# Kernel optimization log

Measured on AMD Instinct MI355X. Metric: run time of the kernel, lower is better.

## Reference

```python
import jax, jax.numpy as jnp
import numpy as np
from jax import lax

COST_BBOX = 1.0  # matcher weight on the L1 bbox cost
INF = jnp.float32(1e9)


def setup_inputs() -> dict:
    key = jax.random.key(0)
    k1, k2 = jax.random.split(key)
    # [bs, num_queries, 2] predicted point coords, [bs, num_targets, 2] gt coords
    outputs = jax.random.uniform(k1, (8, 512, 2), dtype=jnp.float32)
    targets = jax.random.uniform(k2, (8, 256, 2), dtype=jnp.float32)
    return {"outputs": outputs, "targets": targets}


def _hungarian(cost):
    """Jonker-Volgenant / shortest-augmenting-path Hungarian.

    cost: [T, Q] with T <= Q. Assigns each of the T workers (targets) a
    distinct column (query) minimizing total cost. Returns
    (row_ind [T] sorted query indices, col_ind [T] matched target indices),
    matching scipy.optimize.linear_sum_assignment on cost.T.
    """
    T, Q = cost.shape
    u0 = jnp.zeros((T,), cost.dtype)            # worker potentials
    v0 = jnp.zeros((Q + 1,), cost.dtype)        # column potentials (+1 virtual col)
    p0 = jnp.full((Q + 1,), -1, jnp.int32)      # p[j] = worker assigned to column j

    def assign_one(i, carry):
        u, v, p = carry
        p = p.at[Q].set(i)                      # virtual column holds current worker
        init = (jnp.int32(Q), u, v, p,
                jnp.full((Q,), INF, cost.dtype),  # minv: tentative reduced dists
                jnp.zeros((Q + 1,), bool),        # used columns
                jnp.zeros((Q,), jnp.int32))       # way: predecessor column

        def cond(st):
            j0, _, _, p, _, _, _ = st
            return p[j0] != -1

        def body(st):
            j0, u, v, p, minv, used, way = st
            used = used.at[j0].set(True)
            i0 = p[j0]
            cur = cost[i0] - u[i0] - v[:Q]
            better = (cur < minv) & (~used[:Q])
            minv = jnp.where(better, cur, minv)
            way = jnp.where(better, j0, way)
            masked = jnp.where(used[:Q], INF, minv)
            j1 = jnp.argmin(masked).astype(jnp.int32)
            delta = masked[j1]
            uf = used.astype(cost.dtype)
            u = u.at[jnp.where(used, p, T)].add(delta * uf, mode="drop")
            v = v - delta * uf
            minv = jnp.where(used[:Q], minv, minv - delta)
            return (j1, u, v, p, minv, used, way)

        j0, u, v, p, minv, used, way = lax.while_loop(cond, body, init)

        # augment along the alternating path back to the virtual column
        def aug_cond(st):
            j0, _ = st
            return j0 != Q

        def aug_body(st):
            j0, p = st
            j1 = way[j0]
            p = p.at[j0].set(p[j1])
            return (j1, p)

        _, p = lax.while_loop(aug_cond, aug_body, (j0, p))
        return (u, v, p)

    _, _, p = lax.fori_loop(0, T, assign_one, (u0, v0, p0))
    pq = p[:Q]                                  # target assigned to each query (-1 if none)
    valid = pq >= 0
    # invert: query index assigned to each target (each valid target appears once)
    qr = jnp.zeros((T,), jnp.int32).at[jnp.where(valid, pq, T)].add(
        jnp.arange(Q, dtype=jnp.int32), mode="drop")
    order = jnp.argsort(qr)
    return qr[order], order.astype(jnp.int32)


def reference(outputs, targets):
    # L1 cost matrix: [bs, Q, T]
    C = COST_BBOX * jnp.abs(outputs[:, :, None, :] - targets[:, None, :, :]).sum(-1)
    row_ind, col_ind = jax.vmap(lambda c: _hungarian(c.T))(C)
    return (row_ind, col_ind, C)
```

## Files before the change

kernel.cpp:

```cpp
#include <hip/hip_runtime.h>

#define QN 512
#define TN 256
#define INFV 1000000000.0f

typedef unsigned long long u64;

#if defined(__has_builtin)
#if __has_builtin(__builtin_amdgcn_inverse_ballot_w64)
#define IBAL(m) __builtin_amdgcn_inverse_ballot_w64(m)
#endif
#endif
#ifndef IBAL
#define IBAL(m) ((bool)(((m) >> l) & 1ull))
#endif

__global__ __launch_bounds__(256) void cost_kernel(const float2* __restrict__ outputs,
                                                   const float2* __restrict__ targets,
                                                   float* __restrict__ C) {
    const int t = threadIdx.x;
    const int q = blockIdx.x;
    const int b = blockIdx.y;
    float2 o = outputs[b * QN + q];
    float2 g = targets[b * TN + t];
    C[(size_t)(b * QN + q) * TN + t] = fabsf(o.x - g.x) + fabsf(o.y - g.y);
}

__device__ __forceinline__ float readlane_f(float v, int lane) {
    return __builtin_bit_cast(float, __builtin_amdgcn_readlane(__builtin_bit_cast(int, v), lane));
}

template <int CTRL>
__device__ __forceinline__ float dppminf(float x) {
    int o = __builtin_amdgcn_update_dpp(0, __builtin_bit_cast(int, x), CTRL, 0xF, 0xF, true);
    return fminf(x, __builtin_bit_cast(float, o));
}

#define K8(X) X(0) X(1) X(2) X(3) X(4) X(5) X(6) X(7)
#define R4(X) X(0) X(1) X(2) X(3)

__global__ __launch_bounds__(64, 1) void hung_kernel(const float2* __restrict__ outputs,
                                                     const float2* __restrict__ targets,
                                                     float* __restrict__ out_row,
                                                     float* __restrict__ out_col) {
    const int b = blockIdx.x;
    const int l = threadIdx.x;

#define DECLR(s) float tx##s, ty##s, u##s, rf##s;
    R4(DECLR)
#define LOADR(s) { float2 g = targets[b * TN + l + 64 * s]; tx##s = g.x; ty##s = g.y; u##s = 0.0f; }
    R4(LOADR)

#define DECLC(k) float ox##k, oy##k, v##k, minv##k; int way##k, p##k; const int jc##k = l + 64 * k;
    K8(DECLC)
#define LOADC(k) { float2 o = outputs[b * QN + l + 64 * k]; ox##k = o.x; oy##k = o.y; v##k = 0.0f; \
                   p##k = -1; way##k = QN; }
    K8(LOADC)

#define DECLCM(k) u64 cm##k;
    K8(DECLCM)

    for (int i = 0; i < TN; ++i) {
#define INITC(k) minv##k = INFV; cm##k = 0ull;
        K8(INITC)
#define INITRF(s) rf##s = (i == jc##s) ? 1.0f : 0.0f;
        R4(INITRF)

        const int irs = i >> 6, irl = i & 63;
        float ui0, txv, tyv;
        {
            float a0 = (irs & 1) ? u1 : u0,  a1 = (irs & 1) ? u3 : u2;
            float b0 = (irs & 1) ? tx1 : tx0, b1 = (irs & 1) ? tx3 : tx2;
            float c0 = (irs & 1) ? ty1 : ty0, c1 = (irs & 1) ? ty3 : ty2;
            ui0 = readlane_f((irs & 2) ? a1 : a0, irl);
            txv = readlane_f((irs & 2) ? b1 : b0, irl);
            tyv = readlane_f((irs & 2) ? c1 : c0, irl);
        }

        float dprev = 0.0f;
        int j0s = QN;
        int jfree;
        for (;;) {
#define SCAN(k) { const float cost = __builtin_fabsf(ox##k - txv) + __builtin_fabsf(oy##k - tyv); \
                  const float cur  = (cost - ui0) - v##k; \
                  const float tmp  = minv##k - dprev; \
                  const u64 bt2 = __ballot(cur < tmp) & ~cm##k; \
                  minv##k = IBAL(bt2) ? cur : tmp; \
                  way##k  = IBAL(bt2) ? j0s : way##k; }
            K8(SCAN)

            float lmin = fminf(fminf(fminf(minv0, minv1), fminf(minv2, minv3)),
                               fminf(fminf(minv4, minv5), fminf(minv6, minv7)));
            lmin = dppminf<0x121>(lmin);
            lmin = dppminf<0x122>(lmin);
            lmin = dppminf<0x124>(lmin);
            lmin = dppminf<0x128>(lmin);
            lmin = dppminf<0x142>(lmin);
            lmin = dppminf<0x143>(lmin);
            const float delta = readlane_f(lmin, 63);

#define EBAL(k) const u64 e##k = __ballot(minv##k == delta);
            K8(EBAL)
            u64 esel = e7; int kb = 7;
            esel = e6 ? e6 : esel; kb = e6 ? 6 : kb;
            esel = e5 ? e5 : esel; kb = e5 ? 5 : kb;
            esel = e4 ? e4 : esel; kb = e4 ? 4 : kb;
            esel = e3 ? e3 : esel; kb = e3 ? 3 : kb;
            esel = e2 ? e2 : esel; kb = e2 ? 2 : kb;
            esel = e1 ? e1 : esel; kb = e1 ? 1 : kb;
            esel = e0 ? e0 : esel; kb = e0 ? 0 : kb;
            const int j1s = (kb << 6) | (int)__builtin_ctzll(esel);
            const int cslot = j1s >> 6, clane = j1s & 63;

#define UPDU(s) u##s = fmaf(rf##s, delta, u##s);
            R4(UPDU)
#define UPDV(k) { const float vm = v##k - delta; v##k = IBAL(cm##k) ? vm : v##k; }
            K8(UPDV)
            dprev = delta;

            int psel;
            {
                int a0 = (cslot & 1) ? p1 : p0, a1 = (cslot & 1) ? p3 : p2;
                int a2 = (cslot & 1) ? p5 : p4, a3 = (cslot & 1) ? p7 : p6;
                int b0 = (cslot & 2) ? a1 : a0, b1 = (cslot & 2) ? a3 : a2;
                psel = (cslot & 4) ? b1 : b0;
            }
            const int i0s = __builtin_amdgcn_readlane(psel, clane);
            if (i0s < 0) { jfree = j1s; break; }

            const u64 cb = 1ull << clane;
#define MRKC(k) { const u64 mb = (cslot == k) ? cb : 0ull; cm##k |= mb; \
                  minv##k = IBAL(mb) ? INFV : minv##k; }
            K8(MRKC)

            const int nrs = i0s >> 6, nrl = i0s & 63;
            {
                float a0 = (nrs & 1) ? u1 : u0,  a1 = (nrs & 1) ? u3 : u2;
                float b0 = (nrs & 1) ? tx1 : tx0, b1 = (nrs & 1) ? tx3 : tx2;
                float c0 = (nrs & 1) ? ty1 : ty0, c1 = (nrs & 1) ? ty3 : ty2;
                ui0 = readlane_f((nrs & 2) ? a1 : a0, nrl);
                txv = readlane_f((nrs & 2) ? b1 : b0, nrl);
                tyv = readlane_f((nrs & 2) ? c1 : c0, nrl);
            }
#define MARKR(s) rf##s = (i0s == jc##s) ? 1.0f : rf##s;
            R4(MARKR)

            j0s = j1s;
        }

        {
            int jj = jfree;
            for (;;) {
                const int ws = jj >> 6, wl = jj & 63;
                int wsel;
                {
                    int a0 = (ws & 1) ? way1 : way0, a1 = (ws & 1) ? way3 : way2;
                    int a2 = (ws & 1) ? way5 : way4, a3 = (ws & 1) ? way7 : way6;
                    int b0 = (ws & 2) ? a1 : a0, b1 = (ws & 2) ? a3 : a2;
                    wsel = (ws & 4) ? b1 : b0;
                }
                const int jn = __builtin_amdgcn_readlane(wsel, wl);
                int pn;
                if (jn == QN) pn = i;
                else {
                    const int qs = jn >> 6, ql = jn & 63;
                    int qsel;
                    {
                        int a0 = (qs & 1) ? p1 : p0, a1 = (qs & 1) ? p3 : p2;
                        int a2 = (qs & 1) ? p5 : p4, a3 = (qs & 1) ? p7 : p6;
                        int b0 = (qs & 2) ? a1 : a0, b1 = (qs & 2) ? a3 : a2;
                        qsel = (qs & 4) ? b1 : b0;
                    }
                    pn = __builtin_amdgcn_readlane(qsel, ql);
                }
#define SETP(k) p##k = (jj == jc##k) ? pn : p##k;
                K8(SETP)
                if (jn == QN) break;
                jj = jn;
            }
        }
    }

    int rank_base = 0;
#define EMIT(k) { const int pq = p##k; const bool valid = pq >= 0; \
                  u64 m = __ballot(valid); \
                  int below = __popcll(m & ((1ull << l) - 1ull)); \
                  if (valid) { int r = rank_base + below; \
                               out_row[b * TN + r] = (float)jc##k; \
                               out_col[b * TN + r] = (float)pq; } \
                  rank_base += __popcll(m); }
    K8(EMIT)
}

extern "C" void kernel_launch(void* const* d_in, const int* in_sizes, int n_in,
                              void* d_out, int out_size, void* d_ws, size_t ws_size,
                              hipStream_t stream) {
    const float2* outputs = (const float2*)d_in[0];
    const float2* targets = (const float2*)d_in[1];
    float* out = (float*)d_out;
    float* out_row = out;
    float* out_col = out + 8 * TN;
    float* C       = out + 2 * 8 * TN;

    dim3 gridC(QN, 8);
    cost_kernel<<<gridC, TN, 0, stream>>>(outputs, targets, C);
    hung_kernel<<<8, 64, 0, stream>>>(outputs, targets, out_row, out_col);
}
```

Baseline: 358.8 us.

## Pack column state into float2 vectors and byte-packed assignment registers

Per-column state (ox, oy, v, minv, u, rf) is regrouped into 2-wide float vectors so the scan and update steps can use packed FP32 arithmetic. The per-column assignment array p is packed as bytes into two 32-bit registers, and a separate matched-column bitmask per slot replaces the p<0 check. The aim is fewer VALU instructions and lower register pressure in the serial augmenting-path loop, at the cost of extra byte extract/insert work and a dependence on target indices fitting in 8 bits.

After: 383.3 us. 1.07x slower.

```diff
diff --git a/kernel.cpp b/kernel.cpp
--- a/kernel.cpp
+++ b/kernel.cpp
@@ -5,6 +5,7 @@
 #define INFV 1000000000.0f
 
 typedef unsigned long long u64;
+typedef float f32x2 __attribute__((ext_vector_type(2)));
 
 #if defined(__has_builtin)
 #if __has_builtin(__builtin_amdgcn_inverse_ballot_w64)
@@ -37,7 +38,7 @@
 }
 
 #define K8(X) X(0) X(1) X(2) X(3) X(4) X(5) X(6) X(7)
-#define R4(X) X(0) X(1) X(2) X(3)
+#define P4(X) X(0, 0, 1) X(1, 2, 3) X(2, 4, 5) X(3, 6, 7)
 
 __global__ __launch_bounds__(64, 1) void hung_kernel(const float2* __restrict__ outputs,
                                                      const float2* __restrict__ targets,
@@ -46,51 +47,78 @@
     const int b = blockIdx.x;
     const int l = threadIdx.x;
 
-#define DECLR(s) float tx##s, ty##s, u##s, rf##s;
-    R4(DECLR)
-#define LOADR(s) { float2 g = targets[b * TN + l + 64 * s]; tx##s = g.x; ty##s = g.y; u##s = 0.0f; }
-    R4(LOADR)
-
-#define DECLC(k) float ox##k, oy##k, v##k, minv##k; int way##k, p##k; const int jc##k = l + 64 * k;
-    K8(DECLC)
-#define LOADC(k) { float2 o = outputs[b * QN + l + 64 * k]; ox##k = o.x; oy##k = o.y; v##k = 0.0f; \
-                   p##k = -1; way##k = QN; }
-    K8(LOADC)
-
-#define DECLCM(k) u64 cm##k;
-    K8(DECLCM)
+    f32x2 uP0 = {0.0f, 0.0f}, uP1 = {0.0f, 0.0f}, rfP0, rfP1;
+    float tx0, tx1, tx2, tx3, ty0, ty1, ty2, ty3;
+    {
+        float2 g0 = targets[b * TN + l];
+        float2 g1 = targets[b * TN + l + 64];
+        float2 g2 = targets[b * TN + l + 128];
+        float2 g3 = targets[b * TN + l + 192];
+        tx0 = g0.x; ty0 = g0.y; tx1 = g1.x; ty1 = g1.y;
+        tx2 = g2.x; ty2 = g2.y; tx3 = g3.x; ty3 = g3.y;
+    }
+
+    f32x2 oxP0, oxP1, oxP2, oxP3, oyP0, oyP1, oyP2, oyP3;
+    f32x2 vP0, vP1, vP2, vP3, minvP0, minvP1, minvP2, minvP3;
+    int way0, way1, way2, way3, way4, way5, way6, way7;
+    unsigned pA = 0u, pB = 0u;
+#define LOADP(q, ka, kb) { \
+        float2 oa = outputs[b * QN + l + 64 * ka]; \
+        float2 ob = outputs[b * QN + l + 64 * kb]; \
+        oxP##q = (f32x2){oa.x, ob.x}; oyP##q = (f32x2){oa.y, ob.y}; \
+        vP##q = (f32x2){0.0f, 0.0f}; \
+        way##ka = QN; way##kb = QN; }
+    P4(LOADP)
+
+#define DECLM(k) u64 mm##k = 0ull;
+    K8(DECLM)
 
     for (int i = 0; i < TN; ++i) {
-#define INITC(k) minv##k = INFV; cm##k = 0ull;
-        K8(INITC)
-#define INITRF(s) rf##s = (i == jc##s) ? 1.0f : 0.0f;
-        R4(INITRF)
+#define INITP(q, ka, kb) minvP##q = (f32x2){INFV, INFV};
+        P4(INITP)
+#define DECLCM(k) u64 cm##k = 0ull;
+        K8(DECLCM)
 
         const int irs = i >> 6, irl = i & 63;
+        {
+            const u64 rbm = 1ull << irl;
+            rfP0.x = IBAL((irs == 0) ? rbm : 0ull) ? 1.0f : 0.0f;
+            rfP0.y = IBAL((irs == 1) ? rbm : 0ull) ? 1.0f : 0.0f;
+            rfP1.x = IBAL((irs == 2) ? rbm : 0ull) ? 1.0f : 0.0f;
+            rfP1.y = IBAL((irs == 3) ? rbm : 0ull) ? 1.0f : 0.0f;
+        }
         float ui0, txv, tyv;
         {
-            float a0 = (irs & 1) ? u1 : u0,  a1 = (irs & 1) ? u3 : u2;
-            float b0 = (irs & 1) ? tx1 : tx0, b1 = (irs & 1) ? tx3 : tx2;
-            float c0 = (irs & 1) ? ty1 : ty0, c1 = (irs & 1) ? ty3 : ty2;
-            ui0 = readlane_f((irs & 2) ? a1 : a0, irl);
-            txv = readlane_f((irs & 2) ? b1 : b0, irl);
-            tyv = readlane_f((irs & 2) ? c1 : c0, irl);
+            f32x2 up = (irs & 2) ? uP1 : uP0;
+            ui0 = readlane_f((irs & 1) ? up.y : up.x, irl);
+            float ta = (irs & 1) ? tx1 : tx0, tb = (irs & 1) ? tx3 : tx2;
+            txv = readlane_f((irs & 2) ? tb : ta, irl);
+            float ya = (irs & 1) ? ty1 : ty0, yb = (irs & 1) ? ty3 : ty2;
+            tyv = readlane_f((irs & 2) ? yb : ya, irl);
         }
 
         float dprev = 0.0f;
         int j0s = QN;
         int jfree;
         for (;;) {
-#define SCAN(k) { const float cost = __builtin_fabsf(ox##k - txv) + __builtin_fabsf(oy##k - tyv); \
-                  const float cur  = (cost - ui0) - v##k; \
-                  const float tmp  = minv##k - dprev; \
-                  const u64 bt2 = __ballot(cur < tmp) & ~cm##k; \
-                  minv##k = IBAL(bt2) ? cur : tmp; \
-                  way##k  = IBAL(bt2) ? j0s : way##k; }
-            K8(SCAN)
-
-            float lmin = fminf(fminf(fminf(minv0, minv1), fminf(minv2, minv3)),
-                               fminf(fminf(minv4, minv5), fminf(minv6, minv7)));
+#define SCANP(q, ka, kb) { \
+            f32x2 d1 = oxP##q - txv; \
+            f32x2 d2 = oyP##q - tyv; \
+            f32x2 cost = __builtin_elementwise_abs(d1) + __builtin_elementwise_abs(d2); \
+            f32x2 cur = (cost - ui0) - vP##q; \
+            f32x2 tmp = minvP##q - dprev; \
+            const u64 bta = __ballot(cur.x < tmp.x) & ~cm##ka; \
+            const u64 btb = __ballot(cur.y < tmp.y) & ~cm##kb; \
+            minvP##q.x = IBAL(bta) ? cur.x : tmp.x; \
+            minvP##q.y = IBAL(btb) ? cur.y : tmp.y; \
+            way##ka = IBAL(bta) ? j0s : way##ka; \
+            way##kb = IBAL(btb) ? j0s : way##kb; }
+            P4(SCANP)
+
+            f32x2 m01 = __builtin_elementwise_min(minvP0, minvP1);
+            f32x2 m23 = __builtin_elementwise_min(minvP2, minvP3);
+            f32x2 mp  = __builtin_elementwise_min(m01, m23);
+            float lmin = fminf(mp.x, mp.y);
             lmin = dppminf<0x121>(lmin);
             lmin = dppminf<0x122>(lmin);
             lmin = dppminf<0x124>(lmin);
@@ -99,52 +127,73 @@
             lmin = dppminf<0x143>(lmin);
             const float delta = readlane_f(lmin, 63);
 
-#define EBAL(k) const u64 e##k = __ballot(minv##k == delta);
-            K8(EBAL)
-            u64 esel = e7; int kb = 7;
-            esel = e6 ? e6 : esel; kb = e6 ? 6 : kb;
-            esel = e5 ? e5 : esel; kb = e5 ? 5 : kb;
-            esel = e4 ? e4 : esel; kb = e4 ? 4 : kb;
-            esel = e3 ? e3 : esel; kb = e3 ? 3 : kb;
-            esel = e2 ? e2 : esel; kb = e2 ? 2 : kb;
-            esel = e1 ? e1 : esel; kb = e1 ? 1 : kb;
-            esel = e0 ? e0 : esel; kb = e0 ? 0 : kb;
-            const int j1s = (kb << 6) | (int)__builtin_ctzll(esel);
+            const u64 e0 = __ballot(minvP0.x == delta);
+            const u64 e1 = __ballot(minvP0.y == delta);
+            const u64 e2 = __ballot(minvP1.x == delta);
+            const u64 e3 = __ballot(minvP1.y == delta);
+            const u64 e4 = __ballot(minvP2.x == delta);
+            const u64 e5 = __ballot(minvP2.y == delta);
+            const u64 e6 = __ballot(minvP3.x == delta);
+            const u64 e7 = __ballot(minvP3.y == delta);
+            u64 esel = e7; int kb_ = 7;
+            esel = e6 ? e6 : esel; kb_ = e6 ? 6 : kb_;
+            esel = e5 ? e5 : esel; kb_ = e5 ? 5 : kb_;
+            esel = e4 ? e4 : esel; kb_ = e4 ? 4 : kb_;
+            esel = e3 ? e3 : esel; kb_ = e3 ? 3 : kb_;
+            esel = e2 ? e2 : esel; kb_ = e2 ? 2 : kb_;
+            esel = e1 ? e1 : esel; kb_ = e1 ? 1 : kb_;
+            esel = e0 ? e0 : esel; kb_ = e0 ? 0 : kb_;
+            const int j1s = (kb_ << 6) | (int)__builtin_ctzll(esel);
             const int cslot = j1s >> 6, clane = j1s & 63;
 
-#define UPDU(s) u##s = fmaf(rf##s, delta, u##s);
-            R4(UPDU)
-#define UPDV(k) { const float vm = v##k - delta; v##k = IBAL(cm##k) ? vm : v##k; }
-            K8(UPDV)
+            const f32x2 dl2 = {delta, delta};
+            uP0 = __builtin_elementwise_fma(rfP0, dl2, uP0);
+            uP1 = __builtin_elementwise_fma(rfP1, dl2, uP1);
+#define UPDVP(q, ka, kb) { f32x2 vm = vP##q - delta; \
+            vP##q.x = IBAL(cm##ka) ? vm.x : vP##q.x; \
+            vP##q.y = IBAL(cm##kb) ? vm.y : vP##q.y; }
+            P4(UPDVP)
             dprev = delta;
 
-            int psel;
-            {
-                int a0 = (cslot & 1) ? p1 : p0, a1 = (cslot & 1) ? p3 : p2;
-                int a2 = (cslot & 1) ? p5 : p4, a3 = (cslot & 1) ? p7 : p6;
-                int b0 = (cslot & 2) ? a1 : a0, b1 = (cslot & 2) ? a3 : a2;
-                psel = (cslot & 4) ? b1 : b0;
-            }
-            const int i0s = __builtin_amdgcn_readlane(psel, clane);
-            if (i0s < 0) { jfree = j1s; break; }
+            u64 mmsel = mm0;
+            mmsel = (cslot == 1) ? mm1 : mmsel;
+            mmsel = (cslot == 2) ? mm2 : mmsel;
+            mmsel = (cslot == 3) ? mm3 : mmsel;
+            mmsel = (cslot == 4) ? mm4 : mmsel;
+            mmsel = (cslot == 5) ? mm5 : mmsel;
+            mmsel = (cslot == 6) ? mm6 : mmsel;
+            mmsel = (cslot == 7) ? mm7 : mmsel;
+            if (((mmsel >> clane) & 1ull) == 0ull) { jfree = j1s; break; }
+
+            const unsigned pwA = (unsigned)__builtin_amdgcn_readlane((int)pA, clane);
+            const unsigned pwB = (unsigned)__builtin_amdgcn_readlane((int)pB, clane);
+            const unsigned pws = (cslot & 4) ? pwB : pwA;
+            const int i0s = (int)((pws >> ((cslot & 3) * 8)) & 0xFFu);
 
             const u64 cb = 1ull << clane;
-#define MRKC(k) { const u64 mb = (cslot == k) ? cb : 0ull; cm##k |= mb; \
-                  minv##k = IBAL(mb) ? INFV : minv##k; }
-            K8(MRKC)
+#define MRKC0(k, href) { const u64 mb = (cslot == k) ? cb : 0ull; cm##k |= mb; \
+                         href = IBAL(mb) ? INFV : href; }
+            MRKC0(0, minvP0.x) MRKC0(1, minvP0.y)
+            MRKC0(2, minvP1.x) MRKC0(3, minvP1.y)
+            MRKC0(4, minvP2.x) MRKC0(5, minvP2.y)
+            MRKC0(6, minvP3.x) MRKC0(7, minvP3.y)
 
             const int nrs = i0s >> 6, nrl = i0s & 63;
             {
-                float a0 = (nrs & 1) ? u1 : u0,  a1 = (nrs & 1) ? u3 : u2;
-                float b0 = (nrs & 1) ? tx1 : tx0, b1 = (nrs & 1) ? tx3 : tx2;
-                float c0 = (nrs & 1) ? ty1 : ty0, c1 = (nrs & 1) ? ty3 : ty2;
-                ui0 = readlane_f((nrs & 2) ? a1 : a0, nrl);
-                txv = readlane_f((nrs & 2) ? b1 : b0, nrl);
-                tyv = readlane_f((nrs & 2) ? c1 : c0, nrl);
+                f32x2 up = (nrs & 2) ? uP1 : uP0;
+                ui0 = readlane_f((nrs & 1) ? up.y : up.x, nrl);
+                float ta = (nrs & 1) ? tx1 : tx0, tb = (nrs & 1) ? tx3 : tx2;
+                txv = readlane_f((nrs & 2) ? tb : ta, nrl);
+                float ya = (nrs & 1) ? ty1 : ty0, yb = (nrs & 1) ? ty3 : ty2;
+                tyv = readlane_f((nrs & 2) ? yb : ya, nrl);
             }
-#define MARKR(s) rf##s = (i0s == jc##s) ? 1.0f : rf##s;
-            R4(MARKR)
-
+            {
+                const u64 rbm = 1ull << nrl;
+                rfP0.x = IBAL((nrs == 0) ? rbm : 0ull) ? 1.0f : rfP0.x;
+                rfP0.y = IBAL((nrs == 1) ? rbm : 0ull) ? 1.0f : rfP0.y;
+                rfP1.x = IBAL((nrs == 2) ? rbm : 0ull) ? 1.0f : rfP1.x;
+                rfP1.y = IBAL((nrs == 3) ? rbm : 0ull) ? 1.0f : rfP1.y;
+            }
             j0s = j1s;
         }
 
@@ -164,30 +213,37 @@
                 if (jn == QN) pn = i;
                 else {
                     const int qs = jn >> 6, ql = jn & 63;
-                    int qsel;
-                    {
-                        int a0 = (qs & 1) ? p1 : p0, a1 = (qs & 1) ? p3 : p2;
-                        int a2 = (qs & 1) ? p5 : p4, a3 = (qs & 1) ? p7 : p6;
-                        int b0 = (qs & 2) ? a1 : a0, b1 = (qs & 2) ? a3 : a2;
-                        qsel = (qs & 4) ? b1 : b0;
-                    }
-                    pn = __builtin_amdgcn_readlane(qsel, ql);
+                    const unsigned qwA = (unsigned)__builtin_amdgcn_readlane((int)pA, ql);
+                    const unsigned qwB = (unsigned)__builtin_amdgcn_readlane((int)pB, ql);
+                    const unsigned qws = (qs & 4) ? qwB : qwA;
+                    pn = (int)((qws >> ((qs & 3) * 8)) & 0xFFu);
                 }
-#define SETP(k) p##k = (jj == jc##k) ? pn : p##k;
-                K8(SETP)
+                const int sh = (ws & 3) * 8;
+                const unsigned bm = 0xFFu << sh;
+                const unsigned bv = ((unsigned)pn) << sh;
+                const u64 lm_ = 1ull << wl;
+                const u64 mA_ = (ws < 4) ? lm_ : 0ull;
+                const u64 mB_ = (ws < 4) ? 0ull : lm_;
+                pA = IBAL(mA_) ? ((pA & ~bm) | bv) : pA;
+                pB = IBAL(mB_) ? ((pB & ~bm) | bv) : pB;
                 if (jn == QN) break;
                 jj = jn;
             }
+            const int fs = jfree >> 6;
+            const u64 fb = 1ull << (jfree & 63);
+#define SETM(k) mm##k = (fs == k) ? (mm##k | fb) : mm##k;
+            K8(SETM)
         }
     }
 
     int rank_base = 0;
-#define EMIT(k) { const int pq = p##k; const bool valid = pq >= 0; \
-                  u64 m = __ballot(valid); \
-                  int below = __popcll(m & ((1ull << l) - 1ull)); \
-                  if (valid) { int r = rank_base + below; \
-                               out_row[b * TN + r] = (float)jc##k; \
-                               out_col[b * TN + r] = (float)pq; } \
+#define EMIT(k) { const u64 m = mm##k; \
+                  const int below = __popcll(m & ((1ull << l) - 1ull)); \
+                  if (IBAL(m)) { const int r = rank_base + below; \
+                      const unsigned pw = (k < 4) ? pA : pB; \
+                      const int pq = (int)((pw >> ((k & 3) * 8)) & 0xFFu); \
+                      out_row[b * TN + r] = (float)(l + 64 * k); \
+                      out_col[b * TN + r] = (float)pq; } \
                   rank_base += __popcll(m); }
     K8(EMIT)
 }
```

## Fuse cost-matrix computation into the Hungarian kernel launch

Applied to the files above, without the earlier changes.

Merges the separate cost kernel and the Hungarian kernel into one launch. The first 8 blocks run the serial Hungarian solver and the remaining blocks compute the L1 cost matrix with float4 vector stores. This removes one kernel launch and lets the cost writes overlap the long-running solver blocks. It also narrows the scope of the column-mask variables and reshapes the local min tree, which may change register allocation in the hot loop.

Result: no change. 353.6 us (-1.5%).

```diff
diff --git a/kernel.cpp b/kernel.cpp
--- a/kernel.cpp
+++ b/kernel.cpp
@@ -15,17 +15,6 @@
 #define IBAL(m) ((bool)(((m) >> l) & 1ull))
 #endif
 
-__global__ __launch_bounds__(256) void cost_kernel(const float2* __restrict__ outputs,
-                                                   const float2* __restrict__ targets,
-                                                   float* __restrict__ C) {
-    const int t = threadIdx.x;
-    const int q = blockIdx.x;
-    const int b = blockIdx.y;
-    float2 o = outputs[b * QN + q];
-    float2 g = targets[b * TN + t];
-    C[(size_t)(b * QN + q) * TN + t] = fabsf(o.x - g.x) + fabsf(o.y - g.y);
-}
-
 __device__ __forceinline__ float readlane_f(float v, int lane) {
     return __builtin_bit_cast(float, __builtin_amdgcn_readlane(__builtin_bit_cast(int, v), lane));
 }
@@ -39,12 +28,33 @@
 #define K8(X) X(0) X(1) X(2) X(3) X(4) X(5) X(6) X(7)
 #define R4(X) X(0) X(1) X(2) X(3)
 
-__global__ __launch_bounds__(64, 1) void hung_kernel(const float2* __restrict__ outputs,
-                                                     const float2* __restrict__ targets,
-                                                     float* __restrict__ out_row,
-                                                     float* __restrict__ out_col) {
+__global__ __launch_bounds__(64, 1) void fused_kernel(const float2* __restrict__ outputs,
+                                                      const float2* __restrict__ targets,
+                                                      float* __restrict__ out_row,
+                                                      float* __restrict__ out_col,
+                                                      float* __restrict__ C) {
+    const int l = threadIdx.x;
+
+    if (blockIdx.x >= 8) {
+        const int cb = blockIdx.x - 8;
+        const int q  = cb & (QN - 1);
+        const int b  = cb >> 9;
+        const float2 o = outputs[b * QN + q];
+        const int t0 = l * 4;
+        const float2 g0 = targets[b * TN + t0 + 0];
+        const float2 g1 = targets[b * TN + t0 + 1];
+        const float2 g2 = targets[b * TN + t0 + 2];
+        const float2 g3 = targets[b * TN + t0 + 3];
+        float4 r;
+        r.x = fabsf(o.x - g0.x) + fabsf(o.y - g0.y);
+        r.y = fabsf(o.x - g1.x) + fabsf(o.y - g1.y);
+        r.z = fabsf(o.x - g2.x) + fabsf(o.y - g2.y);
+        r.w = fabsf(o.x - g3.x) + fabsf(o.y - g3.y);
+        *reinterpret_cast<float4*>(&C[(size_t)(b * QN + q) * TN + t0]) = r;
+        return;
+    }
+
     const int b = blockIdx.x;
-    const int l = threadIdx.x;
 
 #define DECLR(s) float tx##s, ty##s, u##s, rf##s;
     R4(DECLR)
@@ -57,12 +67,11 @@
                    p##k = -1; way##k = QN; }
     K8(LOADC)
 
-#define DECLCM(k) u64 cm##k;
-    K8(DECLCM)
-
     for (int i = 0; i < TN; ++i) {
-#define INITC(k) minv##k = INFV; cm##k = 0ull;
+#define INITC(k) minv##k = INFV;
         K8(INITC)
+#define DECLCM(k) u64 cm##k = 0ull;
+        K8(DECLCM)
 #define INITRF(s) rf##s = (i == jc##s) ? 1.0f : 0.0f;
         R4(INITRF)
 
@@ -89,8 +98,10 @@
                   way##k  = IBAL(bt2) ? j0s : way##k; }
             K8(SCAN)
 
-            float lmin = fminf(fminf(fminf(minv0, minv1), fminf(minv2, minv3)),
-                               fminf(fminf(minv4, minv5), fminf(minv6, minv7)));
+            const float t0_ = fminf(fminf(minv0, minv1), minv2);
+            const float t1_ = fminf(fminf(minv3, minv4), minv5);
+            const float t2_ = fminf(fminf(minv6, minv7), t0_);
+            float lmin = fminf(t1_, t2_);
             lmin = dppminf<0x121>(lmin);
             lmin = dppminf<0x122>(lmin);
             lmin = dppminf<0x124>(lmin);
@@ -128,8 +139,8 @@
             const int i0s = __builtin_amdgcn_readlane(psel, clane);
             if (i0s < 0) { jfree = j1s; break; }
 
-            const u64 cb = 1ull << clane;
-#define MRKC(k) { const u64 mb = (cslot == k) ? cb : 0ull; cm##k |= mb; \
+            const u64 cb_ = 1ull << clane;
+#define MRKC(k) { const u64 mb = (cslot == k) ? cb_ : 0ull; cm##k |= mb; \
                   minv##k = IBAL(mb) ? INFV : minv##k; }
             K8(MRKC)
 
@@ -202,7 +213,6 @@
     float* out_col = out + 8 * TN;
     float* C       = out + 2 * 8 * TN;
 
-    dim3 gridC(QN, 8);
-    cost_kernel<<<gridC, TN, 0, stream>>>(outputs, targets, C);
-    hung_kernel<<<8, 64, 0, stream>>>(outputs, targets, out_row, out_col);
-}
+    fused_kernel<<<8 + 8 * QN * TN / 256, 64, 0, stream>>>(outputs, targets,
+                                                           out_row, out_col, C);
+}
```
